# Optimization experiments

Hardware: AMD Instinct MI355X
Metric: run time of the kernel (lower is better)

The kernel has to match this reference:

```python
import jax, jax.numpy as jnp
import numpy as np

B, N, H = 2048, 5, 5
IN, HID, OUT = 7, 2048, 512  # IN = 1 + c + c^2 with c = (H-1)//2 = 2


def setup_inputs() -> dict:
    key = jax.random.key(0)
    ks = jax.random.split(key, 7)
    k_in = 1.0 / np.sqrt(IN).astype(np.float32)
    k_h = 1.0 / np.sqrt(HID).astype(np.float32)
    return {
        "ins": jax.random.normal(ks[0], (B, N, H, H), jnp.float32),
        "w1": (jax.random.uniform(ks[1], (4, HID, IN), jnp.float32) - 0.5) * k_in,
        "b1": (jax.random.uniform(ks[2], (HID,), jnp.float32) - 0.5) * k_in,
        "w2": (jax.random.uniform(ks[3], (4, HID, HID), jnp.float32) - 0.5) * k_h,
        "b2": (jax.random.uniform(ks[4], (HID,), jnp.float32) - 0.5) * k_h,
        "w3": (jax.random.uniform(ks[5], (4, OUT, HID), jnp.float32) - 0.5) * k_h,
        "b3": (jax.random.uniform(ks[6], (OUT,), jnp.float32) - 0.5) * k_h,
        "ln_g": jnp.ones((HID,), jnp.float32),
        "ln_b": jnp.zeros((HID,), jnp.float32),
    }


def _rot90(x):
    # matches torch: x.flip(3).permute(0,1,3,2)
    return jnp.swapaxes(jnp.flip(x, axis=3), 2, 3)


def _orbit_stack(x):
    b, n = x.shape[0], x.shape[1]
    c = (x.shape[-1] - 1) // 2  # = 2 for H=5
    center = x[:, :, c, c]  # (B,N)
    parts = []
    xi = x
    for _ in range(4):  # fixed C4 group orbit, not a data loop
        parts.append(xi[:, :, :c, :c + 1].reshape(b, n, -1))  # (B,N,c+c^2)
        xi = _rot90(xi)
    orb = jnp.stack(parts, axis=-1)  # (B,N,c+c^2,4)
    cen = jnp.broadcast_to(center[..., None, None], (b, n, 1, 4))
    out = jnp.concatenate([cen, orb], axis=2)  # (B,N,n_orbits,4)
    return jnp.transpose(out, (0, 1, 3, 2))  # (B,N,4,n_orbits)


def _c4conv(w, bias, x):
    # block-circulant kernel: mat[g,h] = w[(h-g) % 4]
    mat = jnp.stack([jnp.roll(w, i, axis=0) for i in range(4)], axis=0)  # (4,4,out,in)
    return jnp.einsum('ghij,bnhj->bngi', mat, x) + bias


def _layernorm(x, g, b, eps=1e-5):
    m = jnp.mean(x, axis=-1, keepdims=True)
    v = jnp.mean(jnp.square(x - m), axis=-1, keepdims=True)
    return (x - m) / jnp.sqrt(v + eps) * g + b


def reference(ins, w1, b1, w2, b2, w3, b3, ln_g, ln_b):
    h = _orbit_stack(ins)                          # (B,N,4,7)
    h = jax.nn.relu(_c4conv(w1, b1, h))            # (B,N,4,HID)
    h = jax.nn.relu(_layernorm(_c4conv(w2, b2, h), ln_g, ln_b))
    return _c4conv(w3, b3, h)                      # (B,N,4,OUT)
```

## Files before the change

### kernel.cpp

```cpp
#include <hip/hip_runtime.h>
#include <stdint.h>


#define HID 2048
#define MROWS 10240

typedef float floatx4 __attribute__((ext_vector_type(4)));
typedef __bf16 bf16x8 __attribute__((ext_vector_type(8)));

__device__ __forceinline__ unsigned short f2bf(float f) {
  union { float f; unsigned int u; } v; v.f = f;
  unsigned int r = v.u + 0x7fffu + ((v.u >> 16) & 1u);
  return (unsigned short)(r >> 16);
}
__device__ __forceinline__ float bf2f(unsigned short s) {
  union { unsigned int u; float f; } v; v.u = ((unsigned int)s) << 16;
  return v.f;
}

template <int NO>
__global__ __launch_bounds__(256) void wtrans_kernel(const float* __restrict__ w,
                                                     unsigned short* __restrict__ W0s,
                                                     unsigned short* __restrict__ W2s,
                                                     unsigned short* __restrict__ Bc) {
  int idx = blockIdx.x * 256 + threadIdx.x;
  int i = idx >> 9, j4 = idx & 511;
  const float4* wp = (const float4*)w;
  float4 w0 = wp[0 * NO * 512 + i * 512 + j4];
  float4 w1 = wp[1 * NO * 512 + i * 512 + j4];
  float4 w2 = wp[2 * NO * 512 + i * 512 + j4];
  float4 w3 = wp[3 * NO * 512 + i * 512 + j4];
  ushort4 s0, s2, vr, vi, nvi;
#define DO(c)                                        \
  s0.c = f2bf(w0.c + w1.c + w2.c + w3.c);            \
  s2.c = f2bf(w0.c - w1.c + w2.c - w3.c);            \
  vr.c = f2bf(w0.c - w2.c);                          \
  vi.c = f2bf(w1.c - w3.c);                          \
  nvi.c = f2bf(-(w1.c - w3.c));
  DO(x) DO(y) DO(z) DO(w)
#undef DO
  ((ushort4*)W0s)[i * 512 + j4] = s0;
  ((ushort4*)W2s)[i * 512 + j4] = s2;
  ((ushort4*)Bc)[i * 1024 + j4] = vr;
  ((ushort4*)Bc)[i * 1024 + 512 + j4] = nvi;
  ((ushort4*)Bc)[(NO + i) * 1024 + j4] = vi;
  ((ushort4*)Bc)[(NO + i) * 1024 + 512 + j4] = vr;
}

__global__ __launch_bounds__(256) void layer1_kernel(const float* __restrict__ ins,
                                                     const float* __restrict__ w1,
                                                     const float* __restrict__ b1,
                                                     unsigned short* __restrict__ h1s,
                                                     int row0) {
  __shared__ float orbs[32][28];
  int t = threadIdx.x;
  int b0 = blockIdx.x * 32;
  int i = blockIdx.y * 256 + t;
  if (t < 32) {
    const float* x = ins + (size_t)(row0 + b0 + t) * 25;
    float v[25];
#pragma unroll
    for (int p = 0; p < 25; ++p) v[p] = x[p];
    float* o = orbs[t];
    o[0] = v[12]; o[7] = v[12]; o[14] = v[12]; o[21] = v[12];
#pragma unroll
    for (int r = 0; r < 2; ++r)
#pragma unroll
      for (int c = 0; c < 3; ++c) {
        int m = 1 + r * 3 + c;
        o[m]      = v[r * 5 + c];
        o[7 + m]  = v[c * 5 + (4 - r)];
        o[14 + m] = v[(4 - r) * 5 + (4 - c)];
        o[21 + m] = v[(4 - c) * 5 + r];
      }
  }
  __syncthreads();
  float w[4][7];
#pragma unroll
  for (int r = 0; r < 4; ++r)
#pragma unroll
    for (int j = 0; j < 7; ++j) w[r][j] = w1[(r * HID + i) * 7 + j];
  float bias = b1[i];
  for (int s = 0; s < 32; ++s) {
    float a[4] = {bias, bias, bias, bias};
#pragma unroll
    for (int hh = 0; hh < 4; ++hh)
#pragma unroll
      for (int j = 0; j < 7; ++j) {
        float ov = orbs[s][hh * 7 + j];
#pragma unroll
        for (int g = 0; g < 4; ++g) a[g] += w[(hh - g) & 3][j] * ov;
      }
    float h0 = fmaxf(a[0], 0.f), h1 = fmaxf(a[1], 0.f);
    float h2 = fmaxf(a[2], 0.f), h3 = fmaxf(a[3], 0.f);
    size_t base = (size_t)(b0 + s) * 8192 + i;
    h1s[base]        = f2bf(h0 + h1 + h2 + h3);
    h1s[base + 2048] = f2bf(h0 - h1 + h2 - h3);
    h1s[base + 4096] = f2bf(h0 - h2);
    h1s[base + 6144] = f2bf(h3 - h1);
  }
}


__global__ __launch_bounds__(512, 2) void gemm_spec(const unsigned short* __restrict__ A,
                                                    const unsigned short* __restrict__ B0,
                                                    const unsigned short* __restrict__ B1,
                                                    const unsigned short* __restrict__ B2,
                                                    float* __restrict__ Cf,
                                                    unsigned short* __restrict__ Cb,
                                                    int s1, int s2, int N0, int ldc,
                                                    int NT, int NTL, int MTN) {
  __shared__ __align__(16) unsigned short As[2][16384];
  __shared__ __align__(16) unsigned short Bs[2][16384];
  int tid = threadIdx.x;
  int wave = tid >> 6, lane = tid & 63;
  int lane15 = lane & 15, lane4 = lane >> 4, l7 = lane15 & 7;
  int wm = wave >> 2, wn = wave & 3;
  int wm64 = wm << 6, wn32 = wn << 5;

  int srow = tid >> 3;
  int scol = ((tid & 7) ^ ((tid >> 3) & 7)) << 3;
  int bs64 = (srow >> 5) << 6;

#define STA(buf, mh, kk)                                                                              \
  __builtin_amdgcn_global_load_lds(                                                                   \
      (const __attribute__((address_space(1))) void*)(Agb + (size_t)((mh) * 64) * 8192 + (kk)),       \
      (__attribute__((address_space(3))) void*)((char*)As[buf] + (mh) * 16384 + wave * 1024),         \
      16, 0, 0);                                                                                      \
  __builtin_amdgcn_global_load_lds(                                                                   \
      (const __attribute__((address_space(1))) void*)(Agb + (size_t)((mh) * 64 + 128) * 8192 + (kk)), \
      (__attribute__((address_space(3))) void*)((char*)As[buf] + (mh) * 16384 + 8192 + wave * 1024),  \
      16, 0, 0)

#define STB(buf, nh, kk)                                                                              \
  __builtin_amdgcn_global_load_lds(                                                                   \
      (const __attribute__((address_space(1))) void*)(Bgb + (size_t)(bs64 + (nh) * 32) * ldb + (kk)), \
      (__attribute__((address_space(3))) void*)((char*)Bs[buf] + (nh) * 16384 + wave * 1024),         \
      16, 0, 0);                                                                                      \
  __builtin_amdgcn_global_load_lds(                                                                   \
      (const __attribute__((address_space(1))) void*)(Bgb + (size_t)(bs64 + 128 + (nh) * 32) * ldb + (kk)), \
      (__attribute__((address_space(3))) void*)((char*)Bs[buf] + (nh) * 16384 + 8192 + wave * 1024),  \
      16, 0, 0)

#define RAF(buf, mh)                                                                                  \
  _Pragma("unroll") for (int mi_ = 0; mi_ < 4; ++mi_)                                                 \
  _Pragma("unroll") for (int ks_ = 0; ks_ < 2; ++ks_)                                                 \
      af[mi_][ks_] = *(const bf16x8*)((const char*)As[buf] +                                          \
          (((mh) * 128 + wm64 + mi_ * 16 + lane15) << 7) + (((ks_ * 4 + lane4) ^ l7) << 4))

#define RBF(dst, buf, nh)                                                                             \
  _Pragma("unroll") for (int ni_ = 0; ni_ < 2; ++ni_)                                                 \
  _Pragma("unroll") for (int ks_ = 0; ks_ < 2; ++ks_)                                                 \
      dst[ni_][ks_] = *(const bf16x8*)((const char*)Bs[buf] +                                         \
          (((nh) * 128 + wn32 + ni_ * 16 + lane15) << 7) + (((ks_ * 4 + lane4) ^ l7) << 4))

#define MM(mh, nh, bF)                                                                                \
  _Pragma("unroll") for (int mi_ = 0; mi_ < 4; ++mi_)                                                 \
  _Pragma("unroll") for (int ni_ = 0; ni_ < 2; ++ni_)                                                 \
  _Pragma("unroll") for (int ks_ = 0; ks_ < 2; ++ks_)                                                 \
      acc[(mh) * 4 + mi_][(nh) * 2 + ni_] = __builtin_amdgcn_mfma_f32_16x16x32_bf16(                  \
          af[mi_][ks_], bF[ni_][ks_], acc[(mh) * 4 + mi_][(nh) * 2 + ni_], 0, 0, 0)

#define BAR() __builtin_amdgcn_s_barrier()
#define LGKM0() asm volatile("s_waitcnt lgkmcnt(0)" ::: "memory")
#define LGKM8() asm volatile("s_waitcnt lgkmcnt(8)" ::: "memory")
#define VM6() asm volatile("s_waitcnt vmcnt(6)" ::: "memory")

  bf16x8 af[4][2], b0r[2][2], b1r[2][2];
  const floatx4 fz = {0.f, 0.f, 0.f, 0.f};
  floatx4 acc[8][4];

  int G = (int)gridDim.x;
  for (int pass = 0;; ++pass) {
    int base = pass * G;
    if (base >= NT) break;
    int wt = (pass & 1) ? (base + G - 1 - (int)blockIdx.x) : (base + (int)blockIdx.x);
    if (wt >= NT) continue;

    int mt, nt;
    if (wt < NTL) { int j = wt / MTN; nt = s2 + j; mt = wt - j * MTN; }
    else          { int w2_ = wt - NTL; int j = w2_ / MTN; nt = j; mt = w2_ - j * MTN; }
    int m0 = mt * 256;

    const unsigned short* Bp;
    int K, aoff, coff, nloc;
    if (nt < s1)      { Bp = B0; K = 2048; aoff = 0;    coff = 0;      nloc = nt * 256; }
    else if (nt < s2) { Bp = B1; K = 2048; aoff = 2048; coff = N0;     nloc = (nt - s1) * 256; }
    else              { Bp = B2; K = 4096; aoff = 4096; coff = 2 * N0; nloc = (nt - s2) * 256; }
    int ldb = K;

    const unsigned short* Agb = A + (size_t)(m0 + srow) * 8192 + aoff + scol;
    const unsigned short* Bgb = Bp + (size_t)(nloc + (srow & 31)) * ldb + scol;

#pragma unroll
    for (int a = 0; a < 8; ++a)
#pragma unroll
      for (int b = 0; b < 4; ++b) acc[a][b] = fz;

    STA(0, 0, 0); STB(0, 0, 0); STB(0, 1, 0); STA(0, 1, 0);
    STA(1, 0, 64); STB(1, 0, 64); STB(1, 1, 64);
    VM6();
    BAR();

    for (int k0 = 0; k0 < K; k0 += 128) {
      RAF(0, 0); RBF(b0r, 0, 0);
      STA(1, 1, k0 + 64);
      LGKM8();
      BAR(); LGKM0();
      __builtin_amdgcn_s_setprio(1); MM(0, 0, b0r); __builtin_amdgcn_s_setprio(0);
      BAR();
      RBF(b1r, 0, 1);
      STA(0, 0, k0 + 128);
      BAR(); LGKM0();
      __builtin_amdgcn_s_setprio(1); MM(0, 1, b1r); __builtin_amdgcn_s_setprio(0);
      BAR();
      RAF(0, 1);
      STB(0, 0, k0 + 128);
      BAR(); LGKM0();
      __builtin_amdgcn_s_setprio(1); MM(1, 0, b0r); __builtin_amdgcn_s_setprio(0);
      BAR();
      STB(0, 1, k0 + 128);
      BAR(); LGKM0();
      __builtin_amdgcn_s_setprio(1); MM(1, 1, b1r); __builtin_amdgcn_s_setprio(0);
      VM6();
      BAR();
      RAF(1, 0); RBF(b0r, 1, 0);
      STA(0, 1, k0 + 128);
      LGKM8();
      BAR(); LGKM0();
      __builtin_amdgcn_s_setprio(1); MM(0, 0, b0r); __builtin_amdgcn_s_setprio(0);
      BAR();
      RBF(b1r, 1, 1);
      STA(1, 0, k0 + 192);
      BAR(); LGKM0();
      __builtin_amdgcn_s_setprio(1); MM(0, 1, b1r); __builtin_amdgcn_s_setprio(0);
      BAR();
      RAF(1, 1);
      STB(1, 0, k0 + 192);
      BAR(); LGKM0();
      __builtin_amdgcn_s_setprio(1); MM(1, 0, b0r); __builtin_amdgcn_s_setprio(0);
      BAR();
      STB(1, 1, k0 + 192);
      BAR(); LGKM0();
      __builtin_amdgcn_s_setprio(1); MM(1, 1, b1r); __builtin_amdgcn_s_setprio(0);
      VM6();
      BAR();
    }
    asm volatile("s_waitcnt vmcnt(0)" ::: "memory");

#pragma unroll
    for (int ni = 0; ni < 4; ++ni) {
      int col = coff + nloc + wn * 64 + (ni >> 1) * 32 + (ni & 1) * 16 + lane15;
#pragma unroll
      for (int mi = 0; mi < 8; ++mi) {
        int row = m0 + wm * 128 + (mi >> 2) * 64 + (mi & 3) * 16 + lane4 * 4;
        if (Cb) {
#pragma unroll
          for (int r = 0; r < 4; ++r)
            Cb[(size_t)(row + r) * ldc + col] = f2bf(acc[mi][ni][r]);
        } else {
#pragma unroll
          for (int r = 0; r < 4; ++r)
            Cf[(size_t)(row + r) * ldc + col] = acc[mi][ni][r];
        }
      }
    }
  }
#undef STA
#undef STB
#undef RAF
#undef RBF
#undef MM
#undef BAR
#undef LGKM0
#undef LGKM8
#undef VM6
}

__global__ __launch_bounds__(256) void ln_spec_kernel(const unsigned short* C2,
                                                      const float* __restrict__ b2,
                                                      const float* __restrict__ ln_g,
                                                      const float* __restrict__ ln_b,
                                                      unsigned short* h1s) {
  int t = threadIdx.x;
  size_t base = (size_t)blockIdx.x * 8192;
  const ushort4* p = (const ushort4*)(C2 + base);
  const float4* bp2 = (const float4*)b2;
  float4 y[4][2];
  float s[4] = {0, 0, 0, 0}, q[4] = {0, 0, 0, 0};
#pragma unroll
  for (int hl = 0; hl < 2; ++hl) {
    int j = hl * 256 + t;
    ushort4 u0 = p[j], u2 = p[512 + j], ur = p[1024 + j], ui = p[1536 + j];
    float4 bb = bp2[j];
#define DO(c)                                                   \
  {                                                             \
    float v0 = bf2f(u0.c), v2 = bf2f(u2.c);                     \
    float vr = bf2f(ur.c), vi = bf2f(ui.c);                     \
    float e0 = 0.25f * (v0 + v2 + 2.f * vr) + bb.c;             \
    float e1 = 0.25f * (v0 - v2 - 2.f * vi) + bb.c;             \
    float e2 = 0.25f * (v0 + v2 - 2.f * vr) + bb.c;             \
    float e3 = 0.25f * (v0 - v2 + 2.f * vi) + bb.c;             \
    y[0][hl].c = e0; y[1][hl].c = e1; y[2][hl].c = e2; y[3][hl].c = e3; \
    s[0] += e0; q[0] += e0 * e0; s[1] += e1; q[1] += e1 * e1;   \
    s[2] += e2; q[2] += e2 * e2; s[3] += e3; q[3] += e3 * e3;   \
  }
    DO(x) DO(y) DO(z) DO(w)
#undef DO
  }
#pragma unroll
  for (int off = 32; off > 0; off >>= 1)
#pragma unroll
    for (int g = 0; g < 4; ++g) {
      s[g] += __shfl_down(s[g], off, 64);
      q[g] += __shfl_down(q[g], off, 64);
    }
  __shared__ float rs[4][4], rq[4][4];
  int w = t >> 6, l = t & 63;
  if (l == 0)
#pragma unroll
    for (int g = 0; g < 4; ++g) { rs[w][g] = s[g]; rq[w][g] = q[g]; }
  __syncthreads();
  float mean[4], rstd[4];
#pragma unroll
  for (int g = 0; g < 4; ++g) {
    float ss = rs[0][g] + rs[1][g] + rs[2][g] + rs[3][g];
    float qq = rq[0][g] + rq[1][g] + rq[2][g] + rq[3][g];
    mean[g] = ss * (1.f / HID);
    float var = qq * (1.f / HID) - mean[g] * mean[g];
    rstd[g] = rsqrtf(var + 1e-5f);
  }
  const float4* gp = (const float4*)ln_g;
  const float4* lbp = (const float4*)ln_b;
#pragma unroll
  for (int hl = 0; hl < 2; ++hl) {
    int j = hl * 256 + t;
    float4 gg = gp[j], lb = lbp[j];
    ushort4 o[4];
#define DO(c)                                                               \
  {                                                                         \
    float h0 = fmaxf((y[0][hl].c - mean[0]) * rstd[0] * gg.c + lb.c, 0.f);  \
    float h1 = fmaxf((y[1][hl].c - mean[1]) * rstd[1] * gg.c + lb.c, 0.f);  \
    float h2 = fmaxf((y[2][hl].c - mean[2]) * rstd[2] * gg.c + lb.c, 0.f);  \
    float h3 = fmaxf((y[3][hl].c - mean[3]) * rstd[3] * gg.c + lb.c, 0.f);  \
    o[0].c = f2bf(h0 + h1 + h2 + h3);                                       \
    o[1].c = f2bf(h0 - h1 + h2 - h3);                                       \
    o[2].c = f2bf(h0 - h2);                                                 \
    o[3].c = f2bf(h3 - h1);                                                 \
  }
    DO(x) DO(y) DO(z) DO(w)
#undef DO
    size_t ob = (size_t)blockIdx.x * 8192;
#pragma unroll
    for (int pl = 0; pl < 4; ++pl)
      ((ushort4*)(h1s + ob + pl * 2048))[j] = o[pl];
  }
}

__global__ __launch_bounds__(256) void out_ep_kernel(const float* __restrict__ Z,
                                                     const float* __restrict__ b3,
                                                     float* __restrict__ out) {
  int e = blockIdx.x * 256 + threadIdx.x;
  int row = e >> 9, i = e & 511;
  size_t base = (size_t)row * 2048;
  float z0 = Z[base + i], z2 = Z[base + 512 + i];
  float zr = Z[base + 1024 + i], zi = Z[base + 1536 + i];
  float bv = b3[i];
  out[base + i]        = 0.25f * (z0 + z2 + 2.f * zr) + bv;
  out[base + 512 + i]  = 0.25f * (z0 - z2 - 2.f * zi) + bv;
  out[base + 1024 + i] = 0.25f * (z0 + z2 - 2.f * zr) + bv;
  out[base + 1536 + i] = 0.25f * (z0 - z2 + 2.f * zi) + bv;
}

extern "C" void kernel_launch(void* const* d_in, const int* in_sizes, int n_in,
                              void* d_out, int out_size, void* d_ws, size_t ws_size,
                              hipStream_t stream) {
  const float* ins = (const float*)d_in[0];
  const float* w1  = (const float*)d_in[1];
  const float* b1  = (const float*)d_in[2];
  const float* w2  = (const float*)d_in[3];
  const float* b2  = (const float*)d_in[4];
  const float* w3  = (const float*)d_in[5];
  const float* b3  = (const float*)d_in[6];
  const float* lng = (const float*)d_in[7];
  const float* lnb = (const float*)d_in[8];
  float* out = (float*)d_out;
  char* ws = (char*)d_ws;

  unsigned short* W0s2 = (unsigned short*)ws;
  unsigned short* W2s2 = W0s2 + 4194304;
  unsigned short* Bc2  = W2s2 + 4194304;
  unsigned short* W0s3 = Bc2 + 16777216;
  unsigned short* W2s3 = W0s3 + 1048576;
  unsigned short* Bc3  = W2s3 + 1048576;
  const size_t WT_BYTES = 62914560ull;
  char* chunk_base = ws + WT_BYTES;

  wtrans_kernel<2048><<<4096, 256, 0, stream>>>(w2, W0s2, W2s2, Bc2);
  wtrans_kernel<512><<<1024, 256, 0, stream>>>(w3, W0s3, W2s3, Bc3);

  const size_t H1_BYTES = (size_t)5120 * 8192 * 2;
  const size_t H2_BYTES = (size_t)MROWS * 8192 * 2;
  const size_t need_full = WT_BYTES + H1_BYTES + H2_BYTES + 4096;

  if (ws_size >= need_full) {
    unsigned short* h1s = (unsigned short*)chunk_base;
    float*          Z   = (float*)chunk_base;
    unsigned short* H2  = (unsigned short*)(chunk_base + H1_BYTES);
    const int Mc = 5120, MTN = Mc / 256;
    for (int c = 0; c < 2; ++c) {
      int row0 = c * Mc;
      unsigned short* H2c = H2 + (size_t)row0 * 8192;
      layer1_kernel<<<dim3(Mc / 32, 8), 256, 0, stream>>>(ins, w1, b1, h1s, row0);
      gemm_spec<<<256, 512, 0, stream>>>(h1s, W0s2, W2s2, Bc2, nullptr, H2c,
                                         8, 16, 2048, 8192, 32 * MTN, 16 * MTN, MTN);
      ln_spec_kernel<<<Mc, 256, 0, stream>>>(H2c, b2, lng, lnb, H2c);
    }
    {
      const int MT3 = MROWS / 256;
      gemm_spec<<<256, 512, 0, stream>>>(H2, W0s3, W2s3, Bc3, Z, nullptr,
                                         2, 4, 512, 2048, 8 * MT3, 4 * MT3, MT3);
      out_ep_kernel<<<MROWS * 2, 256, 0, stream>>>(Z, b3, out);
    }
  } else {
    static const int Pcand[8] = {1, 2, 4, 5, 8, 10, 20, 40};
    int P = 40;
    for (int pi = 0; pi < 8; ++pi) {
      size_t mc = (size_t)MROWS / Pcand[pi];
      size_t need = WT_BYTES + mc * 8192 * 2 * 2 + 4096;
      if (need <= ws_size) { P = Pcand[pi]; break; }
    }
    const int Mc = MROWS / P, MTN = Mc / 256;
    unsigned short* h1s = (unsigned short*)chunk_base;
    unsigned short* C2  = (unsigned short*)(chunk_base + (size_t)Mc * 8192 * 2);
    float*          Z   = (float*)C2;
    for (int c = 0; c < P; ++c) {
      int row0 = c * Mc;
      layer1_kernel<<<dim3(Mc / 32, 8), 256, 0, stream>>>(ins, w1, b1, h1s, row0);
      gemm_spec<<<256, 512, 0, stream>>>(h1s, W0s2, W2s2, Bc2, nullptr, C2,
                                         8, 16, 2048, 8192, 32 * MTN, 16 * MTN, MTN);
      ln_spec_kernel<<<Mc, 256, 0, stream>>>(C2, b2, lng, lnb, h1s);
      gemm_spec<<<256, 512, 0, stream>>>(h1s, W0s3, W2s3, Bc3, Z, nullptr,
                                         2, 4, 512, 2048, 8 * MTN, 4 * MTN, MTN);
      out_ep_kernel<<<Mc * 2, 256, 0, stream>>>(Z, b3, out + (size_t)row0 * 2048);
    }
  }
}
```

Before: 1.001 ms.

## Reorder GEMM A-tile prefetch, use nontemporal epilogue stores, vectorize output epilogue

The GEMM prologue now issues the fourth A sub-tile load up front (waiting with vmcnt(8)) and moves the in-loop load of that sub-tile to the end of the iteration, so the prefetch sits further ahead of its use. GEMM output stores become nontemporal to reduce cache pollution. The output epilogue kernel is rewritten to process float4 vectors, with four times fewer blocks. The reordering risks incorrect vmcnt accounting if the counts no longer match outstanding loads.

```diff
diff --git a/kernel.cpp b/kernel.cpp
--- a/kernel.cpp
+++ b/kernel.cpp
@@ -165,6 +165,7 @@
 #define LGKM0() asm volatile("s_waitcnt lgkmcnt(0)" ::: "memory")
 #define LGKM8() asm volatile("s_waitcnt lgkmcnt(8)" ::: "memory")
 #define VM6() asm volatile("s_waitcnt vmcnt(6)" ::: "memory")
+#define VM8() asm volatile("s_waitcnt vmcnt(8)" ::: "memory")
 
   bf16x8 af[4][2], b0r[2][2], b1r[2][2];
   const floatx4 fz = {0.f, 0.f, 0.f, 0.f};
@@ -198,13 +199,12 @@
       for (int b = 0; b < 4; ++b) acc[a][b] = fz;
 
     STA(0, 0, 0); STB(0, 0, 0); STB(0, 1, 0); STA(0, 1, 0);
-    STA(1, 0, 64); STB(1, 0, 64); STB(1, 1, 64);
-    VM6();
+    STA(1, 0, 64); STB(1, 0, 64); STB(1, 1, 64); STA(1, 1, 64);
+    VM8();
     BAR();
 
     for (int k0 = 0; k0 < K; k0 += 128) {
       RAF(0, 0); RBF(b0r, 0, 0);
-      STA(1, 1, k0 + 64);
       LGKM8();
       BAR(); LGKM0();
       __builtin_amdgcn_s_setprio(1); MM(0, 0, b0r); __builtin_amdgcn_s_setprio(0);
@@ -241,6 +241,7 @@
       __builtin_amdgcn_s_setprio(1); MM(1, 0, b0r); __builtin_amdgcn_s_setprio(0);
       BAR();
       STB(1, 1, k0 + 192);
+      STA(1, 1, k0 + 192);
       BAR(); LGKM0();
       __builtin_amdgcn_s_setprio(1); MM(1, 1, b1r); __builtin_amdgcn_s_setprio(0);
       VM6();
@@ -257,11 +258,13 @@
         if (Cb) {
 #pragma unroll
           for (int r = 0; r < 4; ++r)
-            Cb[(size_t)(row + r) * ldc + col] = f2bf(acc[mi][ni][r]);
+            __builtin_nontemporal_store(f2bf(acc[mi][ni][r]),
+                                        &Cb[(size_t)(row + r) * ldc + col]);
         } else {
 #pragma unroll
           for (int r = 0; r < 4; ++r)
-            Cf[(size_t)(row + r) * ldc + col] = acc[mi][ni][r];
+            __builtin_nontemporal_store(acc[mi][ni][r],
+                                        &Cf[(size_t)(row + r) * ldc + col]);
         }
       }
     }
@@ -275,6 +278,7 @@
 #undef LGKM0
 #undef LGKM8
 #undef VM6
+#undef VM8
 }
 
 __global__ __launch_bounds__(256) void ln_spec_kernel(const unsigned short* C2,
@@ -361,15 +365,26 @@
                                                      const float* __restrict__ b3,
                                                      float* __restrict__ out) {
   int e = blockIdx.x * 256 + threadIdx.x;
-  int row = e >> 9, i = e & 511;
-  size_t base = (size_t)row * 2048;
-  float z0 = Z[base + i], z2 = Z[base + 512 + i];
-  float zr = Z[base + 1024 + i], zi = Z[base + 1536 + i];
-  float bv = b3[i];
-  out[base + i]        = 0.25f * (z0 + z2 + 2.f * zr) + bv;
-  out[base + 512 + i]  = 0.25f * (z0 - z2 - 2.f * zi) + bv;
-  out[base + 1024 + i] = 0.25f * (z0 + z2 - 2.f * zr) + bv;
-  out[base + 1536 + i] = 0.25f * (z0 - z2 + 2.f * zi) + bv;
+  int row = e >> 7, i4 = e & 127;
+  const float4* Z4 = (const float4*)Z;
+  const float4* b34 = (const float4*)b3;
+  float4* o4 = (float4*)out;
+  size_t base = (size_t)row * 512;
+  float4 z0 = Z4[base + i4],       z2 = Z4[base + 128 + i4];
+  float4 zr = Z4[base + 256 + i4], zi = Z4[base + 384 + i4];
+  float4 bv = b34[i4];
+  float4 e0, e1, e2, e3;
+#define DO(c)                                     \
+  e0.c = 0.25f * (z0.c + z2.c + 2.f * zr.c) + bv.c; \
+  e1.c = 0.25f * (z0.c - z2.c - 2.f * zi.c) + bv.c; \
+  e2.c = 0.25f * (z0.c + z2.c - 2.f * zr.c) + bv.c; \
+  e3.c = 0.25f * (z0.c - z2.c + 2.f * zi.c) + bv.c;
+  DO(x) DO(y) DO(z) DO(w)
+#undef DO
+  o4[base + i4]       = e0;
+  o4[base + 128 + i4] = e1;
+  o4[base + 256 + i4] = e2;
+  o4[base + 384 + i4] = e3;
 }
 
 extern "C" void kernel_launch(void* const* d_in, const int* in_sizes, int n_in,
@@ -420,7 +435,7 @@
       const int MT3 = MROWS / 256;
       gemm_spec<<<256, 512, 0, stream>>>(H2, W0s3, W2s3, Bc3, Z, nullptr,
                                          2, 4, 512, 2048, 8 * MT3, 4 * MT3, MT3);
-      out_ep_kernel<<<MROWS * 2, 256, 0, stream>>>(Z, b3, out);
+      out_ep_kernel<<<MROWS / 2, 256, 0, stream>>>(Z, b3, out);
     }
   } else {
     static const int Pcand[8] = {1, 2, 4, 5, 8, 10, 20, 40};
@@ -442,7 +457,7 @@
       ln_spec_kernel<<<Mc, 256, 0, stream>>>(C2, b2, lng, lnb, h1s);
       gemm_spec<<<256, 512, 0, stream>>>(h1s, W0s3, W2s3, Bc3, Z, nullptr,
                                          2, 4, 512, 2048, 8 * MTN, 4 * MTN, MTN);
-      out_ep_kernel<<<Mc * 2, 256, 0, stream>>>(Z, b3, out + (size_t)row0 * 2048);
-    }
-  }
-}
+      out_ep_kernel<<<Mc / 2, 256, 0, stream>>>(Z, b3, out + (size_t)row0 * 2048);
+    }
+  }
+}
```

New measurement: 1.107 ms. 1.11x slower.
